# Performance work log

Hardware: AMD Instinct MI355X
Metric: run time of the kernel (lower is better)

The kernel has to match this reference:

```python
import jax, jax.numpy as jnp
import numpy as np

N, C, SI, VI, H, R = 10000, 2, 128, 16, 4, 32
SH, VH = SI // H, VI // H  # 32, 4
EPS = 1e-8

def _vnorm(x, axis):
    # clamped L2 norm, matches _norm_no_nan
    return jnp.sqrt(jnp.clip(jnp.sum(x * x, axis=axis), EPS, None))

def _gvp_full(s, v, wh, ws_w, ws_b, wv, wsv_w, wsv_b):
    # GVP with activations=(silu, sigmoid), vector_gate=True, vi=vo
    vh = jnp.swapaxes(v, -1, -2) @ wh            # [..., 3, h]
    vn = _vnorm(vh, -2)                          # [..., h]
    so = jnp.concatenate([s, vn], -1) @ ws_w + ws_b
    vo = jnp.swapaxes(vh @ wv, -1, -2)           # [..., vo, 3]
    gate = jax.nn.sigmoid(jax.nn.sigmoid(so) @ wsv_w + wsv_b)
    return jax.nn.silu(so), vo * gate[..., None]

def setup_inputs():
    key = jax.random.key(0)
    ks = iter(jax.random.split(key, 40))
    def lin(i, o):
        return jax.random.normal(next(ks), (i, o), jnp.float32) / np.sqrt(i)
    def bias(o):
        return 0.02 * jax.random.normal(next(ks), (o,), jnp.float32)
    inp = {}
    inp['s'] = jax.random.normal(next(ks), (N, C, SI), jnp.float32)
    inp['v'] = jax.random.normal(next(ks), (N, C, VI, 3), jnp.float32)
    # weight_proj: GVP((SI,VI)->(R,0)), no activations; h_dim = max(VI,0) = VI
    inp['wp_wh'] = lin(VI, VI); inp['wp_ws_w'] = lin(VI + SI, R); inp['wp_ws_b'] = bias(R)
    # to_q/k/v: GVP((SI,VI)->(SI,VI)), silu/sigmoid, vector_gate; h_dim = VI
    for p in ('q', 'k', 'vv'):
        inp[p + '_wh'] = lin(VI, VI)
        inp[p + '_ws_w'] = lin(VI + SI, SI); inp[p + '_ws_b'] = bias(SI)
        inp[p + '_wv'] = lin(VI, VI)
        inp[p + '_wsv_w'] = lin(SI, VI); inp[p + '_wsv_b'] = bias(VI)
    # attn_gvp_long: GVP((2*SH, 2*VH) -> (1,0)), no activations; h_dim = 2*VH
    inp['attn_wh'] = lin(2 * VH, 2 * VH)
    inp['attn_ws_w'] = lin(2 * VH + 2 * SH, 1); inp['attn_ws_b'] = bias(1)
    return inp

def reference(s, v, wp_wh, wp_ws_w, wp_ws_b,
              q_wh, q_ws_w, q_ws_b, q_wv, q_wsv_w, q_wsv_b,
              k_wh, k_ws_w, k_ws_b, k_wv, k_wsv_w, k_wsv_b,
              vv_wh, vv_ws_w, vv_ws_b, vv_wv, vv_wsv_w, vv_wsv_b,
              attn_wh, attn_ws_w, attn_ws_b):
    n, c = s.shape[:2]
    # ---- Compress: softmax-pool N -> R anchors ----
    vh = jnp.swapaxes(v, -1, -2) @ wp_wh          # [N,C,3,VI]
    vn = _vnorm(vh, -2)                            # [N,C,VI]
    pw = jnp.concatenate([s, vn], -1) @ wp_ws_w + wp_ws_b  # [N,C,R]
    pw = jax.nn.softmax(pw, axis=0)                # softmax over nodes
    s_g = jnp.einsum('nca,ncs->acs', pw, s)        # [R,C,SI] (includes transpose(0,1))
    v_g = jnp.einsum('nca,ncvd->acvd', pw, v)      # [R,C,VI,3]
    # ---- q from nodes, k/v from anchors ----
    qs, qv = _gvp_full(s, v, q_wh, q_ws_w, q_ws_b, q_wv, q_wsv_w, q_wsv_b)
    ks, kv = _gvp_full(s_g, v_g, k_wh, k_ws_w, k_ws_b, k_wv, k_wsv_w, k_wsv_b)
    vs, vv_ = _gvp_full(s_g, v_g, vv_wh, vv_ws_w, vv_ws_b, vv_wv, vv_wsv_w, vv_wsv_b)
    qs = qs.reshape(n, c, H, SH); qv = qv.reshape(n, c, H, VH, 3)
    ks = ks.reshape(R, c, H, SH); kv = kv.reshape(R, c, H, VH, 3)
    vs = vs.reshape(R, c, H, SH); vv_ = vv_.reshape(R, c, H, VH, 3)
    # ---- attention GVP on cat(q, k): split weights instead of materializing concat ----
    wh_q, wh_k = attn_wh[:VH], attn_wh[VH:]        # wh @ cat(qv,kv) = qv@wh_q + kv@wh_k
    qh = jnp.swapaxes(qv, -1, -2) @ wh_q           # [N,C,H,3,2VH]
    kh = jnp.swapaxes(kv, -1, -2) @ wh_k           # [R,C,H,3,2VH]
    vn2 = _vnorm(qh[:, None] + kh[None], -2)       # [N,R,C,H,2VH]
    ws_q = attn_ws_w[:SH]; ws_k = attn_ws_w[SH:2 * SH]; ws_n = attn_ws_w[2 * SH:]
    e = (qs @ ws_q)[:, None] + (ks @ ws_k)[None] + vn2 @ ws_n + attn_ws_b  # [N,R,C,H,1]
    e = e[..., 0] / np.sqrt(SH)
    alpha = jax.nn.softmax(e, axis=1)              # softmax over anchors (dim=1)
    # ---- Broadcast: weighted sum of anchor values ----
    out_s = jnp.einsum('nrch,rchd->nchd', alpha, vs).reshape(n, c, SI)
    out_v = jnp.einsum('nrch,rchde->nchde', alpha, vv_).reshape(n, c, VI, 3)
    return out_s, out_v
```

## Files before the change

kernel.cpp:

```cpp
#include <hip/hip_runtime.h>
#include <hip/hip_bf16.h>


#define N_  10000
#define C_  2
#define SI_ 128
#define VI_ 16
#define H_  4
#define R_  32
#define SH_ 32
#define VH_ 4
#define NC_ (N_*C_)

typedef const float* __restrict__ fptr;

__device__ __forceinline__ float sigm(float x){ return 1.f/(1.f+__expf(-x)); }

#define OFF_LG  0
#define OFF_EQH 640000
#define OFF_SG  2720000
#define OFF_ST  2731264
#define OFF_TKH 2731392
#define OFF_TEK 2737536
#define OFF_TVS 2737792
#define OFF_TVV 2745984

__global__ __launch_bounds__(256) void kA(
    fptr s, fptr v,
    fptr wp_wh, fptr wp_ws_w, fptr wp_ws_b,
    fptr q_wh, fptr q_ws_w, fptr q_ws_b, fptr q_wv, fptr q_wsv_w, fptr q_wsv_b,
    fptr attn_wh, fptr attn_ws_w,
    float* __restrict__ lg, float* __restrict__ eqh)
{
  __shared__ __align__(16) float ARENA[160*20];
  __shared__ __align__(16) float VVs[16*48];
  __shared__ __align__(16) float VHQ[16*48];
  __shared__ __align__(16) float SO[16*128];
  __shared__ __align__(16) float GATE[16*16];
  __shared__ __align__(16) float QV[16*48];
  float* const XT  = ARENA;
  float* const SIG = ARENA;

  const int tid  = threadIdx.x;
  const int row0 = blockIdx.x * 16;

  for (int idx = tid; idx < 16*128; idx += 256){
    int r = idx >> 7, j = idx & 127;
    XT[j*20 + r] = s[(row0+r)*128 + j];
  }
  for (int idx = tid; idx < 16*48; idx += 256){
    int r = idx / 48, k = idx - r*48;
    VVs[r*48 + k] = v[(row0+r)*48 + k];
  }
  __syncthreads();

  for (int t = tid; t < 512; t += 256){
    int r = t >> 5, ii = t & 31, path = ii >> 4, i = ii & 15;
    fptr wh = path ? wp_wh : q_wh;
    float h0=0.f, h1=0.f, h2=0.f;
    #pragma unroll
    for (int j = 0; j < 16; j++){
      float w = wh[j*16 + i];
      h0 = fmaf(VVs[r*48 + j*3 + 0], w, h0);
      h1 = fmaf(VVs[r*48 + j*3 + 1], w, h1);
      h2 = fmaf(VVs[r*48 + j*3 + 2], w, h2);
    }
    float vn = sqrtf(fmaxf(h0*h0 + h1*h1 + h2*h2, 1e-8f));
    if (!path){
      VHQ[r*48 +  0 + i] = h0;
      VHQ[r*48 + 16 + i] = h1;
      VHQ[r*48 + 32 + i] = h2;
      XT[(128+i)*20 + r] = vn;
    } else {
      XT[(144+i)*20 + r] = vn;
    }
  }
  __syncthreads();

  const int colA = tid & 127, rgA = tid >> 7;
  float acc[8];
  {
    float bqs = q_ws_b[colA];
    #pragma unroll
    for (int k = 0; k < 8; k++) acc[k] = bqs;
    #pragma unroll 4
    for (int j = 0; j < 144; j++){
      float w = q_ws_w[j*128 + colA];
      const float* xp = &XT[j*20 + rgA*8];
      float4 x0 = *(const float4*)xp;
      float4 x1 = *(const float4*)(xp + 4);
      acc[0] = fmaf(x0.x, w, acc[0]); acc[1] = fmaf(x0.y, w, acc[1]);
      acc[2] = fmaf(x0.z, w, acc[2]); acc[3] = fmaf(x0.w, w, acc[3]);
      acc[4] = fmaf(x1.x, w, acc[4]); acc[5] = fmaf(x1.y, w, acc[5]);
      acc[6] = fmaf(x1.z, w, acc[6]); acc[7] = fmaf(x1.w, w, acc[7]);
    }
  }
  {
    const int col = tid & 31, rg = tid >> 5;
    float bp = wp_ws_b[col];
    float a0 = bp, a1 = bp;
    #pragma unroll 4
    for (int j = 0; j < 144; j++){
      int jj = (j < 128) ? j : (j + 16);
      float w = wp_ws_w[j*32 + col];
      const float* xp = &XT[jj*20 + rg*2];
      a0 = fmaf(xp[0], w, a0);
      a1 = fmaf(xp[1], w, a1);
    }
    const int n = (row0 >> 1) + rg;
    lg[(     col)*N_ + n] = a0;
    lg[(32 + col)*N_ + n] = a1;
  }
  __syncthreads();

  #pragma unroll
  for (int k = 0; k < 8; k++){
    float so = acc[k];
    float sg_ = sigm(so);
    SIG[(rgA*8 + k)*128 + colA] = sg_;
    SO [(rgA*8 + k)*128 + colA] = so * sg_;
  }
  __syncthreads();

  {
    const int r = tid >> 4, g = tid & 15;
    float ga = q_wsv_b[g];
    #pragma unroll 8
    for (int o = 0; o < 128; o += 4){
      float4 s4 = *(const float4*)&SIG[r*128 + o];
      ga = fmaf(s4.x, q_wsv_w[(o+0)*16 + g], ga);
      ga = fmaf(s4.y, q_wsv_w[(o+1)*16 + g], ga);
      ga = fmaf(s4.z, q_wsv_w[(o+2)*16 + g], ga);
      ga = fmaf(s4.w, q_wsv_w[(o+3)*16 + g], ga);
    }
    GATE[r*16 + g] = sigm(ga);
  }
  if (tid < 64){
    const int r = tid >> 2, h = tid & 3;
    float e = 0.f;
    #pragma unroll
    for (int t = 0; t < 32; t++)
      e = fmaf(SO[r*128 + h*32 + t], attn_ws_w[t], e);
    eqh[(row0 + r)*104 + h] = e;
  }
  __syncthreads();

  for (int t = tid; t < 16*48; t += 256){
    int r = t / 48, k = t - r*48, i = k / 3, d = k - i*3;
    float a = 0.f;
    #pragma unroll
    for (int j = 0; j < 16; j++)
      a = fmaf(VHQ[r*48 + d*16 + j], q_wv[j*16 + i], a);
    QV[r*48 + k] = a * GATE[r*16 + i];
  }
  __syncthreads();

  for (int t = tid; t < 16*96; t += 256){
    int r = t / 96, k = t - r*96;
    int h = k / 24, rem = k - h*24, d = rem >> 3, ee = rem & 7;
    float a = 0.f;
    #pragma unroll
    for (int i = 0; i < 4; i++)
      a = fmaf(QV[r*48 + (h*4 + i)*3 + d], attn_wh[i*8 + ee], a);
    eqh[(row0 + r)*104 + 8 + k] = a;
  }
}

__global__ __launch_bounds__(256) void kStats(const float* __restrict__ lg,
                                              float* __restrict__ st)
{
  const int q = blockIdx.x;
  const int tid = threadIdx.x;
  const float* col = lg + q*N_;
  __shared__ float red[256];

  float m = -1e30f;
  for (int n = tid; n < N_; n += 256) m = fmaxf(m, col[n]);
  red[tid] = m; __syncthreads();
  for (int s2 = 128; s2 > 0; s2 >>= 1){
    if (tid < s2) red[tid] = fmaxf(red[tid], red[tid + s2]);
    __syncthreads();
  }
  const float mx = red[0];
  __syncthreads();

  float sm = 0.f;
  for (int n = tid; n < N_; n += 256) sm += __expf(col[n] - mx);
  red[tid] = sm; __syncthreads();
  for (int s2 = 128; s2 > 0; s2 >>= 1){
    if (tid < s2) red[tid] += red[tid + s2];
    __syncthreads();
  }
  if (tid == 0){ st[q*2] = mx; st[q*2 + 1] = red[0]; }
}

#define CHUNK_ 50
__global__ __launch_bounds__(256) void kAccum(const float* __restrict__ lg,
                                              const float* __restrict__ st,
                                              fptr s, fptr v,
                                              float* __restrict__ sg)
{
  const int b = blockIdx.x, c = b & 1, chunk = b >> 1;
  const int n0 = chunk * CHUNK_;
  const int tid = threadIdx.x;
  const int ag = tid >> 5, dl = tid & 31;

  float mx[4], dn[4];
  #pragma unroll
  for (int aa = 0; aa < 4; aa++){
    int a = ag*4 + aa;
    mx[aa] = st[(c*32 + a)*2];
    dn[aa] = 1.f / st[(c*32 + a)*2 + 1];
  }
  float acc[4][6] = {};
  for (int n = n0; n < n0 + CHUNK_; n++){
    const int rc = n*2 + c;
    float pw[4];
    #pragma unroll
    for (int aa = 0; aa < 4; aa++)
      pw[aa] = __expf(lg[(c*32 + ag*4 + aa)*N_ + n] - mx[aa]) * dn[aa];
    #pragma unroll
    for (int dd = 0; dd < 6; dd++){
      int d = dl + 32*dd;
      if (d < 176){
        float xv = (d < 128) ? s[rc*128 + d] : v[rc*48 + d - 128];
        #pragma unroll
        for (int aa = 0; aa < 4; aa++)
          acc[aa][dd] = fmaf(pw[aa], xv, acc[aa][dd]);
      }
    }
  }
  #pragma unroll
  for (int aa = 0; aa < 4; aa++)
    #pragma unroll
    for (int dd = 0; dd < 6; dd++){
      int d = dl + 32*dd;
      if (d < 176)
        atomicAdd(&sg[(c*32 + ag*4 + aa)*176 + d], acc[aa][dd]);
    }
}

__global__ __launch_bounds__(256) void kSmall(
    const float* __restrict__ sg,
    fptr k_wh, fptr k_ws_w, fptr k_ws_b, fptr k_wv, fptr k_wsv_w, fptr k_wsv_b,
    fptr vv_wh, fptr vv_ws_w, fptr vv_ws_b, fptr vv_wv, fptr vv_wsv_w, fptr vv_wsv_b,
    fptr attn_wh, fptr attn_ws_w,
    float* __restrict__ tkh, float* __restrict__ tek,
    float* __restrict__ tvs, float* __restrict__ tvv)
{
  const int b = blockIdx.x, r = b >> 1, c = b & 1;
  const int tid = threadIdx.x;
  __shared__ float X[176];
  __shared__ float VN[2][16];
  __shared__ float VH[2][48];
  __shared__ float SOk[128], SOv[128];
  __shared__ float G[2][16];
  __shared__ float KV[48];

  if (tid < 176) X[tid] = sg[(c*32 + r)*176 + tid];
  __syncthreads();

  if (tid < 32){
    int path = tid >> 4, i = tid & 15;
    fptr wh = path ? vv_wh : k_wh;
    float h0=0.f, h1=0.f, h2=0.f;
    #pragma unroll
    for (int j = 0; j < 16; j++){
      float w = wh[j*16 + i];
      h0 = fmaf(X[128 + j*3 + 0], w, h0);
      h1 = fmaf(X[128 + j*3 + 1], w, h1);
      h2 = fmaf(X[128 + j*3 + 2], w, h2);
    }
    VH[path][ 0 + i] = h0; VH[path][16 + i] = h1; VH[path][32 + i] = h2;
    VN[path][i] = sqrtf(fmaxf(h0*h0 + h1*h1 + h2*h2, 1e-8f));
  }
  __syncthreads();

  {
    int path = tid >> 7, col = tid & 127;
    fptr W  = path ? vv_ws_w : k_ws_w;
    fptr Bb = path ? vv_ws_b : k_ws_b;
    float so = Bb[col];
    for (int j = 0; j < 128; j++) so = fmaf(X[j], W[j*128 + col], so);
    #pragma unroll
    for (int i = 0; i < 16; i++)  so = fmaf(VN[path][i], W[(128+i)*128 + col], so);
    (path ? SOv : SOk)[col] = so;
  }
  __syncthreads();

  if (tid < 32){
    int path = tid >> 4, g = tid & 15;
    fptr Wsv = path ? vv_wsv_w : k_wsv_w;
    fptr Bsv = path ? vv_wsv_b : k_wsv_b;
    const float* SOp = path ? SOv : SOk;
    float ga = Bsv[g];
    for (int o = 0; o < 128; o++)
      ga = fmaf(sigm(SOp[o]), Wsv[o*16 + g], ga);
    G[path][g] = sigm(ga);
  } else if (tid < 36){
    int h = tid - 32;
    float e = 0.f;
    #pragma unroll
    for (int t = 0; t < 32; t++){
      float so = SOk[h*32 + t];
      e = fmaf(so * sigm(so), attn_ws_w[32 + t], e);
    }
    tek[(r*2 + c)*4 + h] = e;
  } else if (tid >= 64 && tid < 192){
    int o = tid - 64;
    float so = SOv[o];
    tvs[(r*2 + c)*128 + o] = so * sigm(so);
  }
  __syncthreads();

  if (tid < 96){
    int path = tid / 48, k = tid % 48, i = k / 3, d = k - i*3;
    fptr Wv = path ? vv_wv : k_wv;
    float vo = 0.f;
    #pragma unroll
    for (int j = 0; j < 16; j++)
      vo = fmaf(VH[path][d*16 + j], Wv[j*16 + i], vo);
    float gv = vo * G[path][i];
    if (path == 0) KV[k] = gv;
    else {
      int h = i >> 2, ii = i & 3;
      tvv[(((r*2 + c)*4 + h)*4 + ii)*3 + d] = gv;
    }
  }
  __syncthreads();

  if (tid < 96){
    int h = tid / 24, rem = tid % 24, d = rem >> 3, ee = rem & 7;
    float a = 0.f;
    #pragma unroll
    for (int i = 0; i < 4; i++)
      a = fmaf(KV[(h*4 + i)*3 + d], attn_wh[(4 + i)*8 + ee], a);
    tkh[((r*2 + c)*4 + h)*24 + d*8 + ee] = a;
  }
}

__global__ __launch_bounds__(512) void kAttn(
    const float* __restrict__ eqh,
    const float* __restrict__ tkh, const float* __restrict__ tek,
    const float* __restrict__ tvs, const float* __restrict__ tvv,
    fptr attn_ws_w, fptr attn_ws_b,
    float* __restrict__ out)
{
  __shared__ __align__(16) float KH[6144];
  __shared__ __align__(16) float EK[256];
  __shared__ __align__(16) float VS[256*36];
  __shared__ __align__(16) float VVt[3072];
  const int tid = threadIdx.x;

  for (int i = tid; i < 6144; i += 512) KH[i] = tkh[i];
  if (tid < 256) EK[tid] = tek[tid];
  for (int i = tid; i < 8192; i += 512){ int base = i >> 5, t = i & 31; VS[base*36 + t] = tvs[i]; }
  for (int i = tid; i < 3072; i += 512) VVt[i] = tvv[i];

  float wsn[8];
  #pragma unroll
  for (int ee = 0; ee < 8; ee++) wsn[ee] = attn_ws_w[64 + ee];
  const float wb = attn_ws_b[0];
  __syncthreads();

  const int row = blockIdx.x*128 + (tid >> 2);
  const int h = tid & 3;
  if (row < NC_){
    const int c = row & 1;
    const float eq = eqh[row*104 + h];
    float qh[24];
    const float4* qp = (const float4*)&eqh[row*104 + 8 + h*24];
    #pragma unroll
    for (int k = 0; k < 6; k++){
      float4 t4 = qp[k];
      qh[k*4+0] = t4.x; qh[k*4+1] = t4.y; qh[k*4+2] = t4.z; qh[k*4+3] = t4.w;
    }
    float e[32];
    float em = -1e30f;
    #pragma unroll
    for (int r = 0; r < 32; r++){
      const int base = (r*2 + c)*4 + h;
      const float* khp = &KH[base*24];
      float en = 0.f;
      #pragma unroll
      for (int ee = 0; ee < 8; ee++){
        float a0 = qh[ee]      + khp[ee];
        float a1 = qh[8 + ee]  + khp[8 + ee];
        float a2 = qh[16 + ee] + khp[16 + ee];
        en = fmaf(sqrtf(fmaxf(a0*a0 + a1*a1 + a2*a2, 1e-8f)), wsn[ee], en);
      }
      float ev = (eq + EK[base] + en + wb) * 0.17677669529663687f;
      e[r] = ev; em = fmaxf(em, ev);
    }
    float den = 0.f;
    #pragma unroll
    for (int r = 0; r < 32; r++){ e[r] = __expf(e[r] - em); den += e[r]; }
    const float inv = 1.f / den;
    float accs[32] = {};
    float accv[12] = {};
    #pragma unroll
    for (int r = 0; r < 32; r++){
      const int base = (r*2 + c)*4 + h;
      const float al = e[r] * inv;
      const float* vsp = &VS[base*36];
      #pragma unroll
      for (int t = 0; t < 32; t++) accs[t] = fmaf(al, vsp[t], accs[t]);
      const float* vvp = &VVt[base*12];
      #pragma unroll
      for (int k = 0; k < 12; k++) accv[k] = fmaf(al, vvp[k], accv[k]);
    }
    float* po = &out[row*128 + h*32];
    #pragma unroll
    for (int t = 0; t < 32; t++) po[t] = accs[t];
    float* pv = &out[NC_*128 + row*48 + h*12];
    #pragma unroll
    for (int k = 0; k < 12; k++) pv[k] = accv[k];
  }
}

extern "C" void kernel_launch(void* const* d_in, const int* in_sizes, int n_in,
                              void* d_out, int out_size, void* d_ws, size_t ws_size,
                              hipStream_t stream)
{
  fptr s        = (fptr)d_in[0];
  fptr v        = (fptr)d_in[1];
  fptr wp_wh    = (fptr)d_in[2];
  fptr wp_ws_w  = (fptr)d_in[3];
  fptr wp_ws_b  = (fptr)d_in[4];
  fptr q_wh     = (fptr)d_in[5];
  fptr q_ws_w   = (fptr)d_in[6];
  fptr q_ws_b   = (fptr)d_in[7];
  fptr q_wv     = (fptr)d_in[8];
  fptr q_wsv_w  = (fptr)d_in[9];
  fptr q_wsv_b  = (fptr)d_in[10];
  fptr k_wh     = (fptr)d_in[11];
  fptr k_ws_w   = (fptr)d_in[12];
  fptr k_ws_b   = (fptr)d_in[13];
  fptr k_wv     = (fptr)d_in[14];
  fptr k_wsv_w  = (fptr)d_in[15];
  fptr k_wsv_b  = (fptr)d_in[16];
  fptr vv_wh    = (fptr)d_in[17];
  fptr vv_ws_w  = (fptr)d_in[18];
  fptr vv_ws_b  = (fptr)d_in[19];
  fptr vv_wv    = (fptr)d_in[20];
  fptr vv_wsv_w = (fptr)d_in[21];
  fptr vv_wsv_b = (fptr)d_in[22];
  fptr attn_wh  = (fptr)d_in[23];
  fptr attn_ws_w= (fptr)d_in[24];
  fptr attn_ws_b= (fptr)d_in[25];

  float* ws  = (float*)d_ws;
  float* lg  = ws + OFF_LG;
  float* eqh = ws + OFF_EQH;
  float* sg  = ws + OFF_SG;
  float* st  = ws + OFF_ST;
  float* tkh = ws + OFF_TKH;
  float* tek = ws + OFF_TEK;
  float* tvs = ws + OFF_TVS;
  float* tvv = ws + OFF_TVV;

  hipMemsetAsync(sg, 0, 11264*sizeof(float), stream);

  kA<<<NC_/16, 256, 0, stream>>>(s, v, wp_wh, wp_ws_w, wp_ws_b,
                                 q_wh, q_ws_w, q_ws_b, q_wv, q_wsv_w, q_wsv_b,
                                 attn_wh, attn_ws_w, lg, eqh);
  kStats<<<64, 256, 0, stream>>>(lg, st);
  kAccum<<<2*(N_/CHUNK_), 256, 0, stream>>>(lg, st, s, v, sg);
  kSmall<<<64, 256, 0, stream>>>(sg,
                                 k_wh, k_ws_w, k_ws_b, k_wv, k_wsv_w, k_wsv_b,
                                 vv_wh, vv_ws_w, vv_ws_b, vv_wv, vv_wsv_w, vv_wsv_b,
                                 attn_wh, attn_ws_w, tkh, tek, tvs, tvv);
  kAttn<<<(NC_ + 127)/128, 512, 0, stream>>>(eqh, tkh, tek, tvs, tvv,
                                             attn_ws_w, attn_ws_b, (float*)d_out);
}
```

Measured before the change: 253.2 us.

## Drop softmax stats kernel, normalize pooling late, two rows per thread in attention

The pooling logits are exponentiated directly in kA with no max subtraction, and the denominators are accumulated in kAccum alongside the weighted sums. kSmall then divides by them, which removes the separate kStats reduction kernel. kAttn now uses an online-style pass without a max: each thread handles two rows, reuses the anchor K/V loads from LDS for both, and normalizes at the end. Dropping max subtraction risks overflow for large logits, and the larger per-thread register footprint may lower occupancy.

```diff
diff --git a/kernel.cpp b/kernel.cpp
--- a/kernel.cpp
+++ b/kernel.cpp
@@ -16,21 +16,22 @@
 
 __device__ __forceinline__ float sigm(float x){ return 1.f/(1.f+__expf(-x)); }
 
-#define OFF_LG  0
-#define OFF_EQH 640000
-#define OFF_SG  2720000
-#define OFF_ST  2731264
-#define OFF_TKH 2731392
-#define OFF_TEK 2737536
-#define OFF_TVS 2737792
-#define OFF_TVV 2745984
+#define OFF_LG   0
+#define OFF_EQH  640000
+#define OFF_SG   2640000
+#define OFF_TKH  2651520
+#define OFF_TEK  2657664
+#define OFF_TVS  2657920
+#define OFF_TVV  2666112
+
+#define SGSTRIDE_ 180
 
 __global__ __launch_bounds__(256) void kA(
     fptr s, fptr v,
     fptr wp_wh, fptr wp_ws_w, fptr wp_ws_b,
     fptr q_wh, fptr q_ws_w, fptr q_ws_b, fptr q_wv, fptr q_wsv_w, fptr q_wsv_b,
     fptr attn_wh, fptr attn_ws_w,
-    float* __restrict__ lg, float* __restrict__ eqh)
+    float* __restrict__ pexp, float* __restrict__ eqh)
 {
   __shared__ __align__(16) float ARENA[160*20];
   __shared__ __align__(16) float VVs[16*48];
@@ -108,8 +109,8 @@
       a1 = fmaf(xp[1], w, a1);
     }
     const int n = (row0 >> 1) + rg;
-    lg[(     col)*N_ + n] = a0;
-    lg[(32 + col)*N_ + n] = a1;
+    pexp[(     col)*N_ + n] = __expf(a0);
+    pexp[(32 + col)*N_ + n] = __expf(a1);
   }
   __syncthreads();
 
@@ -141,7 +142,7 @@
     #pragma unroll
     for (int t = 0; t < 32; t++)
       e = fmaf(SO[r*128 + h*32 + t], attn_ws_w[t], e);
-    eqh[(row0 + r)*104 + h] = e;
+    eqh[(row0 + r)*100 + h] = e;
   }
   __syncthreads();
 
@@ -162,66 +163,37 @@
     #pragma unroll
     for (int i = 0; i < 4; i++)
       a = fmaf(QV[r*48 + (h*4 + i)*3 + d], attn_wh[i*8 + ee], a);
-    eqh[(row0 + r)*104 + 8 + k] = a;
+    eqh[(row0 + r)*100 + 8 + k] = a;
   }
 }
 
-__global__ __launch_bounds__(256) void kStats(const float* __restrict__ lg,
-                                              float* __restrict__ st)
-{
-  const int q = blockIdx.x;
-  const int tid = threadIdx.x;
-  const float* col = lg + q*N_;
-  __shared__ float red[256];
-
-  float m = -1e30f;
-  for (int n = tid; n < N_; n += 256) m = fmaxf(m, col[n]);
-  red[tid] = m; __syncthreads();
-  for (int s2 = 128; s2 > 0; s2 >>= 1){
-    if (tid < s2) red[tid] = fmaxf(red[tid], red[tid + s2]);
-    __syncthreads();
-  }
-  const float mx = red[0];
-  __syncthreads();
-
-  float sm = 0.f;
-  for (int n = tid; n < N_; n += 256) sm += __expf(col[n] - mx);
-  red[tid] = sm; __syncthreads();
-  for (int s2 = 128; s2 > 0; s2 >>= 1){
-    if (tid < s2) red[tid] += red[tid + s2];
-    __syncthreads();
-  }
-  if (tid == 0){ st[q*2] = mx; st[q*2 + 1] = red[0]; }
-}
-
-#define CHUNK_ 50
-__global__ __launch_bounds__(256) void kAccum(const float* __restrict__ lg,
-                                              const float* __restrict__ st,
+__global__ __launch_bounds__(256) void kAccum(const float* __restrict__ pexp,
                                               fptr s, fptr v,
                                               float* __restrict__ sg)
 {
-  const int b = blockIdx.x, c = b & 1, chunk = b >> 1;
-  const int n0 = chunk * CHUNK_;
+  const int b = blockIdx.x;
+  const int c = b & 1, ah = (b >> 1) & 1, chunk = b >> 2;
+  const int n0 = chunk * 50;
   const int tid = threadIdx.x;
-  const int ag = tid >> 5, dl = tid & 31;
-
-  float mx[4], dn[4];
-  #pragma unroll
-  for (int aa = 0; aa < 4; aa++){
-    int a = ag*4 + aa;
-    mx[aa] = st[(c*32 + a)*2];
-    dn[aa] = 1.f / st[(c*32 + a)*2 + 1];
-  }
-  float acc[4][6] = {};
-  for (int n = n0; n < n0 + CHUNK_; n++){
+  const int ag = tid >> 6, dl = tid & 63;
+  const int abase = ah*16 + ag*4;
+
+  const float* pb = pexp + (c*32 + abase)*N_;
+  float acc[4][3] = {};
+  float dn[4] = {};
+
+  #pragma unroll 2
+  for (int n = n0; n < n0 + 50; n++){
     const int rc = n*2 + c;
     float pw[4];
     #pragma unroll
-    for (int aa = 0; aa < 4; aa++)
-      pw[aa] = __expf(lg[(c*32 + ag*4 + aa)*N_ + n] - mx[aa]) * dn[aa];
-    #pragma unroll
-    for (int dd = 0; dd < 6; dd++){
-      int d = dl + 32*dd;
+    for (int aa = 0; aa < 4; aa++){
+      pw[aa] = pb[aa*N_ + n];
+      dn[aa] += pw[aa];
+    }
+    #pragma unroll
+    for (int dd = 0; dd < 3; dd++){
+      int d = dl + 64*dd;
       if (d < 176){
         float xv = (d < 128) ? s[rc*128 + d] : v[rc*48 + d - 128];
         #pragma unroll
@@ -231,13 +203,15 @@
     }
   }
   #pragma unroll
-  for (int aa = 0; aa < 4; aa++)
-    #pragma unroll
-    for (int dd = 0; dd < 6; dd++){
-      int d = dl + 32*dd;
-      if (d < 176)
-        atomicAdd(&sg[(c*32 + ag*4 + aa)*176 + d], acc[aa][dd]);
-    }
+  for (int aa = 0; aa < 4; aa++){
+    const int base = (c*32 + abase + aa)*SGSTRIDE_;
+    #pragma unroll
+    for (int dd = 0; dd < 3; dd++){
+      int d = dl + 64*dd;
+      if (d < 176) atomicAdd(&sg[base + d], acc[aa][dd]);
+    }
+    if (dl == 0) atomicAdd(&sg[base + 176], dn[aa]);
+  }
 }
 
 __global__ __launch_bounds__(256) void kSmall(
@@ -257,7 +231,10 @@
   __shared__ float G[2][16];
   __shared__ float KV[48];
 
-  if (tid < 176) X[tid] = sg[(c*32 + r)*176 + tid];
+  if (tid < 176){
+    const float* p = sg + (c*32 + r)*SGSTRIDE_;
+    X[tid] = p[tid] / p[176];
+  }
   __syncthreads();
 
   if (tid < 32){
@@ -339,7 +316,7 @@
   }
 }
 
-__global__ __launch_bounds__(512) void kAttn(
+__global__ __launch_bounds__(256, 1) void kAttn(
     const float* __restrict__ eqh,
     const float* __restrict__ tkh, const float* __restrict__ tek,
     const float* __restrict__ tvs, const float* __restrict__ tvv,
@@ -352,10 +329,10 @@
   __shared__ __align__(16) float VVt[3072];
   const int tid = threadIdx.x;
 
-  for (int i = tid; i < 6144; i += 512) KH[i] = tkh[i];
+  for (int i = tid; i < 6144; i += 256) KH[i] = tkh[i];
   if (tid < 256) EK[tid] = tek[tid];
-  for (int i = tid; i < 8192; i += 512){ int base = i >> 5, t = i & 31; VS[base*36 + t] = tvs[i]; }
-  for (int i = tid; i < 3072; i += 512) VVt[i] = tvv[i];
+  for (int i = tid; i < 8192; i += 256){ int base = i >> 5, t = i & 31; VS[base*36 + t] = tvs[i]; }
+  for (int i = tid; i < 3072; i += 256) VVt[i] = tvv[i];
 
   float wsn[8];
   #pragma unroll
@@ -363,58 +340,109 @@
   const float wb = attn_ws_b[0];
   __syncthreads();
 
-  const int row = blockIdx.x*128 + (tid >> 2);
-  const int h = tid & 3;
-  if (row < NC_){
-    const int c = row & 1;
-    const float eq = eqh[row*104 + h];
-    float qh[24];
-    const float4* qp = (const float4*)&eqh[row*104 + 8 + h*24];
+  const int p = tid >> 2, h = tid & 3;
+  const int q = ((p >> 1) << 2) + (p & 1);
+  const int rowA = blockIdx.x*128 + q;
+  const int rowB = rowA + 2;
+  const int c = q & 1;
+  const bool okA = rowA < NC_, okB = rowB < NC_;
+
+  float qa[24], qb[24];
+  float eqA = 0.f, eqB = 0.f;
+  #pragma unroll
+  for (int k = 0; k < 24; k++){ qa[k] = 0.f; qb[k] = 0.f; }
+  if (okA){
+    eqA = eqh[rowA*100 + h];
+    const float4* qp = (const float4*)&eqh[rowA*100 + 8 + h*24];
     #pragma unroll
     for (int k = 0; k < 6; k++){
       float4 t4 = qp[k];
-      qh[k*4+0] = t4.x; qh[k*4+1] = t4.y; qh[k*4+2] = t4.z; qh[k*4+3] = t4.w;
-    }
-    float e[32];
-    float em = -1e30f;
-    #pragma unroll
-    for (int r = 0; r < 32; r++){
-      const int base = (r*2 + c)*4 + h;
-      const float* khp = &KH[base*24];
-      float en = 0.f;
+      qa[k*4+0]=t4.x; qa[k*4+1]=t4.y; qa[k*4+2]=t4.z; qa[k*4+3]=t4.w;
+    }
+  }
+  if (okB){
+    eqB = eqh[rowB*100 + h];
+    const float4* qp = (const float4*)&eqh[rowB*100 + 8 + h*24];
+    #pragma unroll
+    for (int k = 0; k < 6; k++){
+      float4 t4 = qp[k];
+      qb[k*4+0]=t4.x; qb[k*4+1]=t4.y; qb[k*4+2]=t4.z; qb[k*4+3]=t4.w;
+    }
+  }
+
+  float sa[32], sb[32], va[12], vb[12];
+  #pragma unroll
+  for (int k = 0; k < 32; k++){ sa[k]=0.f; sb[k]=0.f; }
+  #pragma unroll
+  for (int k = 0; k < 12; k++){ va[k]=0.f; vb[k]=0.f; }
+  float denA = 0.f, denB = 0.f;
+
+  #pragma unroll
+  for (int r = 0; r < 32; r++){
+    const int base = (r*2 + c)*4 + h;
+    float kh[24];
+    {
+      const float4* kp4 = (const float4*)&KH[base*24];
       #pragma unroll
-      for (int ee = 0; ee < 8; ee++){
-        float a0 = qh[ee]      + khp[ee];
-        float a1 = qh[8 + ee]  + khp[8 + ee];
-        float a2 = qh[16 + ee] + khp[16 + ee];
-        en = fmaf(sqrtf(fmaxf(a0*a0 + a1*a1 + a2*a2, 1e-8f)), wsn[ee], en);
+      for (int qq = 0; qq < 6; qq++){
+        float4 t4 = kp4[qq];
+        kh[qq*4+0]=t4.x; kh[qq*4+1]=t4.y; kh[qq*4+2]=t4.z; kh[qq*4+3]=t4.w;
       }
-      float ev = (eq + EK[base] + en + wb) * 0.17677669529663687f;
-      e[r] = ev; em = fmaxf(em, ev);
-    }
-    float den = 0.f;
-    #pragma unroll
-    for (int r = 0; r < 32; r++){ e[r] = __expf(e[r] - em); den += e[r]; }
-    const float inv = 1.f / den;
-    float accs[32] = {};
-    float accv[12] = {};
-    #pragma unroll
-    for (int r = 0; r < 32; r++){
-      const int base = (r*2 + c)*4 + h;
-      const float al = e[r] * inv;
-      const float* vsp = &VS[base*36];
-      #pragma unroll
-      for (int t = 0; t < 32; t++) accs[t] = fmaf(al, vsp[t], accs[t]);
-      const float* vvp = &VVt[base*12];
-      #pragma unroll
-      for (int k = 0; k < 12; k++) accv[k] = fmaf(al, vvp[k], accv[k]);
-    }
-    float* po = &out[row*128 + h*32];
-    #pragma unroll
-    for (int t = 0; t < 32; t++) po[t] = accs[t];
-    float* pv = &out[NC_*128 + row*48 + h*12];
-    #pragma unroll
-    for (int k = 0; k < 12; k++) pv[k] = accv[k];
+    }
+    float enA = 0.f, enB = 0.f;
+    #pragma unroll
+    for (int ee = 0; ee < 8; ee++){
+      float a0 = qa[ee] + kh[ee], a1 = qa[8+ee] + kh[8+ee], a2 = qa[16+ee] + kh[16+ee];
+      enA = fmaf(sqrtf(fmaxf(a0*a0 + a1*a1 + a2*a2, 1e-8f)), wsn[ee], enA);
+      float b0 = qb[ee] + kh[ee], b1 = qb[8+ee] + kh[8+ee], b2 = qb[16+ee] + kh[16+ee];
+      enB = fmaf(sqrtf(fmaxf(b0*b0 + b1*b1 + b2*b2, 1e-8f)), wsn[ee], enB);
+    }
+    const float ekv = EK[base];
+    const float wA = okA ? __expf((eqA + ekv + enA + wb) * 0.17677669529663687f) : 0.f;
+    const float wB = okB ? __expf((eqB + ekv + enB + wb) * 0.17677669529663687f) : 0.f;
+    denA += wA; denB += wB;
+
+    const float4* vp4 = (const float4*)&VS[base*36];
+    #pragma unroll
+    for (int qq = 0; qq < 8; qq++){
+      float4 t4 = vp4[qq];
+      sa[qq*4+0] = fmaf(wA, t4.x, sa[qq*4+0]); sb[qq*4+0] = fmaf(wB, t4.x, sb[qq*4+0]);
+      sa[qq*4+1] = fmaf(wA, t4.y, sa[qq*4+1]); sb[qq*4+1] = fmaf(wB, t4.y, sb[qq*4+1]);
+      sa[qq*4+2] = fmaf(wA, t4.z, sa[qq*4+2]); sb[qq*4+2] = fmaf(wB, t4.z, sb[qq*4+2]);
+      sa[qq*4+3] = fmaf(wA, t4.w, sa[qq*4+3]); sb[qq*4+3] = fmaf(wB, t4.w, sb[qq*4+3]);
+    }
+    const float4* vv4 = (const float4*)&VVt[base*12];
+    #pragma unroll
+    for (int qq = 0; qq < 3; qq++){
+      float4 t4 = vv4[qq];
+      va[qq*4+0] = fmaf(wA, t4.x, va[qq*4+0]); vb[qq*4+0] = fmaf(wB, t4.x, vb[qq*4+0]);
+      va[qq*4+1] = fmaf(wA, t4.y, va[qq*4+1]); vb[qq*4+1] = fmaf(wB, t4.y, vb[qq*4+1]);
+      va[qq*4+2] = fmaf(wA, t4.z, va[qq*4+2]); vb[qq*4+2] = fmaf(wB, t4.z, vb[qq*4+2]);
+      va[qq*4+3] = fmaf(wA, t4.w, va[qq*4+3]); vb[qq*4+3] = fmaf(wB, t4.w, vb[qq*4+3]);
+    }
+  }
+
+  if (okA){
+    const float inv = 1.f / denA;
+    float4* po = (float4*)&out[rowA*128 + h*32];
+    #pragma unroll
+    for (int qq = 0; qq < 8; qq++)
+      po[qq] = make_float4(sa[qq*4]*inv, sa[qq*4+1]*inv, sa[qq*4+2]*inv, sa[qq*4+3]*inv);
+    float4* pv = (float4*)&out[NC_*128 + rowA*48 + h*12];
+    #pragma unroll
+    for (int qq = 0; qq < 3; qq++)
+      pv[qq] = make_float4(va[qq*4]*inv, va[qq*4+1]*inv, va[qq*4+2]*inv, va[qq*4+3]*inv);
+  }
+  if (okB){
+    const float inv = 1.f / denB;
+    float4* po = (float4*)&out[rowB*128 + h*32];
+    #pragma unroll
+    for (int qq = 0; qq < 8; qq++)
+      po[qq] = make_float4(sb[qq*4]*inv, sb[qq*4+1]*inv, sb[qq*4+2]*inv, sb[qq*4+3]*inv);
+    float4* pv = (float4*)&out[NC_*128 + rowB*48 + h*12];
+    #pragma unroll
+    for (int qq = 0; qq < 3; qq++)
+      pv[qq] = make_float4(vb[qq*4]*inv, vb[qq*4+1]*inv, vb[qq*4+2]*inv, vb[qq*4+3]*inv);
   }
 }
 
@@ -449,27 +477,25 @@
   fptr attn_ws_w= (fptr)d_in[24];
   fptr attn_ws_b= (fptr)d_in[25];
 
-  float* ws  = (float*)d_ws;
-  float* lg  = ws + OFF_LG;
-  float* eqh = ws + OFF_EQH;
-  float* sg  = ws + OFF_SG;
-  float* st  = ws + OFF_ST;
-  float* tkh = ws + OFF_TKH;
-  float* tek = ws + OFF_TEK;
-  float* tvs = ws + OFF_TVS;
-  float* tvv = ws + OFF_TVV;
-
-  hipMemsetAsync(sg, 0, 11264*sizeof(float), stream);
+  float* ws   = (float*)d_ws;
+  float* pexp = ws + OFF_LG;
+  float* eqh  = ws + OFF_EQH;
+  float* sg   = ws + OFF_SG;
+  float* tkh  = ws + OFF_TKH;
+  float* tek  = ws + OFF_TEK;
+  float* tvs  = ws + OFF_TVS;
+  float* tvv  = ws + OFF_TVV;
+
+  hipMemsetAsync(sg, 0, 64*SGSTRIDE_*sizeof(float), stream);
 
   kA<<<NC_/16, 256, 0, stream>>>(s, v, wp_wh, wp_ws_w, wp_ws_b,
                                  q_wh, q_ws_w, q_ws_b, q_wv, q_wsv_w, q_wsv_b,
-                                 attn_wh, attn_ws_w, lg, eqh);
-  kStats<<<64, 256, 0, stream>>>(lg, st);
-  kAccum<<<2*(N_/CHUNK_), 256, 0, stream>>>(lg, st, s, v, sg);
+                                 attn_wh, attn_ws_w, pexp, eqh);
+  kAccum<<<800, 256, 0, stream>>>(pexp, s, v, sg);
   kSmall<<<64, 256, 0, stream>>>(sg,
                                  k_wh, k_ws_w, k_ws_b, k_wv, k_wsv_w, k_wsv_b,
                                  vv_wh, vv_ws_w, vv_ws_b, vv_wv, vv_wsv_w, vv_wsv_b,
                                  attn_wh, attn_ws_w, tkh, tek, tvs, tvv);
-  kAttn<<<(NC_ + 127)/128, 512, 0, stream>>>(eqh, tkh, tek, tvs, tvv,
+  kAttn<<<(NC_ + 127)/128, 256, 0, stream>>>(eqh, tkh, tek, tvs, tvv,
                                              attn_ws_w, attn_ws_b, (float*)d_out);
 }
```

Result: slower. 684.1 us (+170.2%).
